# Performance work log

Hardware: AMD Instinct MI355X
Metric: run time of the kernel (lower is better)

Reference implementation:

```python
import jax, jax.numpy as jnp
import numpy as np

B, S, HID = 2, 2048, 2304
H, KVH, D = 8, 4, 256          # query heads, kv heads, head_dim
N_REP = H // KVH
SCALE = 256.0 ** -0.5          # query_pre_attn_scalar ** -0.5
SOFTCAP = 50.0
ROPE_THETA = 10000.0
NEG = -1e9


def setup_inputs() -> dict:
    key = jax.random.key(0)
    k1, k2, k3, k4, k5 = jax.random.split(key, 5)
    hidden_states = jax.random.normal(k1, (B, S, HID), dtype=jnp.float32)
    # RoPE cos/sin tables, shape [B, S, D]
    inv_freq = 1.0 / (ROPE_THETA ** (jnp.arange(0, D, 2, dtype=jnp.float32) / D))
    pos = jnp.arange(S, dtype=jnp.float32)
    freqs = pos[:, None] * inv_freq[None, :]            # [S, D/2]
    emb = jnp.concatenate([freqs, freqs], axis=-1)      # [S, D]
    cos = jnp.broadcast_to(jnp.cos(emb)[None], (B, S, D))
    sin = jnp.broadcast_to(jnp.sin(emb)[None], (B, S, D))
    # additive causal mask [B, 1, S, S] (sliding_window=4096 > S, so pure causal)
    idx = jnp.arange(S)
    causal = idx[None, :] <= idx[:, None]
    attention_mask = jnp.broadcast_to(
        jnp.where(causal, 0.0, NEG).astype(jnp.float32)[None, None], (B, 1, S, S))
    # projection weights (lecun-normal-ish scale), no bias (attention_bias=False)
    Wq = jax.random.normal(k2, (HID, H * D), dtype=jnp.float32) / np.sqrt(HID)
    Wk = jax.random.normal(k3, (HID, KVH * D), dtype=jnp.float32) / np.sqrt(HID)
    Wv = jax.random.normal(k4, (HID, KVH * D), dtype=jnp.float32) / np.sqrt(HID)
    Wo = jax.random.normal(k5, (H * D, HID), dtype=jnp.float32) / np.sqrt(H * D)
    return {"hidden_states": hidden_states, "cos": cos, "sin": sin,
            "attention_mask": attention_mask,
            "Wq": Wq, "Wk": Wk, "Wv": Wv, "Wo": Wo}


def _rotate_half(x):
    half = x.shape[-1] // 2
    return jnp.concatenate([-x[..., half:], x[..., :half]], axis=-1)


def reference(hidden_states, cos, sin, attention_mask, Wq, Wk, Wv, Wo):
    b, s, _ = hidden_states.shape
    q = (hidden_states @ Wq).reshape(b, s, H, D).transpose(0, 2, 1, 3)    # [B,H,S,D]
    k = (hidden_states @ Wk).reshape(b, s, KVH, D).transpose(0, 2, 1, 3)  # [B,KVH,S,D]
    v = (hidden_states @ Wv).reshape(b, s, KVH, D).transpose(0, 2, 1, 3)
    c = cos[:, None]  # [B,1,S,D] broadcast over heads (unsqueeze_dim=1)
    sn = sin[:, None]
    q = q * c + _rotate_half(q) * sn
    k = k * c + _rotate_half(k) * sn
    # GQA: repeat kv heads (interleave, matching repeat_kv tile+reshape)
    k = jnp.repeat(k, N_REP, axis=1)
    v = jnp.repeat(v, N_REP, axis=1)
    w = jnp.einsum('bhqd,bhkd->bhqk', q, k) * SCALE
    w = jnp.tanh(w / SOFTCAP) * SOFTCAP                  # logit softcapping
    w = w + attention_mask[:, :, :, :s]
    w = jax.nn.softmax(w.astype(jnp.float32), axis=-1).astype(q.dtype)
    out = jnp.einsum('bhqk,bhkd->bhqd', w, v)
    out = out.transpose(0, 2, 1, 3).reshape(b, s, H * D)
    return out @ Wo
```

## Files before the change

### kernel.cpp

```cpp
#include <hip/hip_runtime.h>

typedef unsigned short u16;
typedef __attribute__((ext_vector_type(8))) short short8;
typedef __attribute__((ext_vector_type(4))) float f32x4;

constexpr int B_ = 2;
constexpr int H_ = 8;
constexpr int KVH_ = 4;
constexpr int S_ = 2048;
constexpr int D_ = 256;
constexpr int HID_ = 2304;
constexpr int QKVN_ = 4096;
constexpr int AON_ = 2048;

__device__ __forceinline__ float b2f(u16 u) {
  union { float f; unsigned int i; } x; x.i = ((unsigned int)u) << 16; return x.f;
}
__device__ __forceinline__ u16 f2b(float f) {
  unsigned int x = __float_as_uint(f);
  unsigned int r = (x + 0x7fffu + ((x >> 16) & 1u)) >> 16;
  return (u16)r;
}

__global__ void cast_kernel(const float* __restrict__ in, u16* __restrict__ out) {
  size_t i = ((size_t)blockIdx.x * 256 + threadIdx.x) * 4;
  float4 v = *(const float4*)(in + i);
  unsigned int lo = (unsigned int)f2b(v.x) | ((unsigned int)f2b(v.y) << 16);
  unsigned int hi = (unsigned int)f2b(v.z) | ((unsigned int)f2b(v.w) << 16);
  uint2 o; o.x = lo; o.y = hi;
  *(uint2*)(out + i) = o;
}

__global__ void transpose_cast(const float* __restrict__ src, u16* __restrict__ dst,
                               int R, int C) {
  __shared__ float tile[64][65];
  int r0 = blockIdx.y * 64, c0 = blockIdx.x * 64;
  int t = threadIdx.x;
#pragma unroll
  for (int i = 0; i < 16; ++i) {
    int e = i * 256 + t;
    int r = e >> 6, c = e & 63;
    tile[r][c] = src[(size_t)(r0 + r) * C + (c0 + c)];
  }
  __syncthreads();
#pragma unroll
  for (int i = 0; i < 16; ++i) {
    int e = i * 256 + t;
    int orow = e >> 6, ocol = e & 63;
    dst[(size_t)(c0 + orow) * R + (r0 + ocol)] = f2b(tile[ocol][orow]);
  }
}

template <int OUTF32>
__global__ __launch_bounds__(256, 2) void gemm_bt(
    const u16* __restrict__ A, const u16* __restrict__ B, void* __restrict__ Cp,
    int M, int N, int K) {
  __shared__ u16 As[128 * 32];
  __shared__ u16 Bs[128 * 32];
  int m0 = blockIdx.y * 128, n0 = blockIdx.x * 128;
  int tid = threadIdx.x;
  int lane = tid & 63, wave = tid >> 6;
  int wy = wave >> 1, wx = wave & 1;
  int quad = lane >> 4, l16 = lane & 15;
  f32x4 acc[4][4] = {};
  for (int k0 = 0; k0 < K; k0 += 32) {
#pragma unroll
    for (int i = 0; i < 2; ++i) {
      int chunk = i * 256 + tid;
      int row = chunk >> 2, col = (chunk & 3) << 3;
      __builtin_amdgcn_global_load_lds(
          (const __attribute__((address_space(1))) void*)(A + (size_t)(m0 + row) * K + k0 + col),
          (__attribute__((address_space(3))) void*)(As + chunk * 8), 16, 0, 0);
    }
#pragma unroll
    for (int i = 0; i < 2; ++i) {
      int chunk = i * 256 + tid;
      int row = chunk >> 2, col = (chunk & 3) << 3;
      __builtin_amdgcn_global_load_lds(
          (const __attribute__((address_space(1))) void*)(B + (size_t)(n0 + row) * K + k0 + col),
          (__attribute__((address_space(3))) void*)(Bs + chunk * 8), 16, 0, 0);
    }
    __syncthreads();
    short8 af[4], bf[4];
#pragma unroll
    for (int mi = 0; mi < 4; ++mi)
      af[mi] = *(const short8*)(As + (wy * 64 + mi * 16 + l16) * 32 + quad * 8);
#pragma unroll
    for (int ni = 0; ni < 4; ++ni)
      bf[ni] = *(const short8*)(Bs + (wx * 64 + ni * 16 + l16) * 32 + quad * 8);
#pragma unroll
    for (int mi = 0; mi < 4; ++mi)
#pragma unroll
      for (int ni = 0; ni < 4; ++ni)
        acc[mi][ni] = __builtin_amdgcn_mfma_f32_16x16x32_bf16(af[mi], bf[ni], acc[mi][ni], 0, 0, 0);
    __syncthreads();
  }
#pragma unroll
  for (int mi = 0; mi < 4; ++mi) {
#pragma unroll
    for (int ni = 0; ni < 4; ++ni) {
#pragma unroll
      for (int r = 0; r < 4; ++r) {
        int row = m0 + wy * 64 + mi * 16 + quad * 4 + r;
        int col = n0 + wx * 64 + ni * 16 + l16;
        if (OUTF32)
          ((float*)Cp)[(size_t)row * N + col] = acc[mi][ni][r];
        else
          ((u16*)Cp)[(size_t)row * N + col] = f2b(acc[mi][ni][r]);
      }
    }
  }
}

__global__ void rope_kernel(const u16* __restrict__ qkv, const float* __restrict__ cs,
                            const float* __restrict__ sn, u16* __restrict__ Qr,
                            u16* __restrict__ Kr) {
  int row = blockIdx.x;
  int b = row >> 11, s = row & 2047;
  int d = threadIdx.x;
  const u16* qrow = qkv + (size_t)row * QKVN_;
  float c = cs[(size_t)row * D_ + d];
  float si = sn[(size_t)row * D_ + d];
  int dp = (d < 128) ? d + 128 : d - 128;
  float sgn = (d < 128) ? -1.f : 1.f;
#pragma unroll
  for (int h = 0; h < H_; ++h) {
    float v = b2f(qrow[h * D_ + d]);
    float p = sgn * b2f(qrow[h * D_ + dp]);
    Qr[((size_t)(b * H_ + h) * S_ + s) * D_ + d] = f2b(v * c + p * si);
  }
#pragma unroll
  for (int g = 0; g < KVH_; ++g) {
    float v = b2f(qrow[2048 + g * D_ + d]);
    float p = sgn * b2f(qrow[2048 + g * D_ + dp]);
    Kr[((size_t)(b * KVH_ + g) * S_ + s) * D_ + d] = f2b(v * c + p * si);
  }
}

__global__ void transpose_v(const u16* __restrict__ qkv, u16* __restrict__ Vt) {
  __shared__ u16 tile[64][72];
  int d0 = blockIdx.x * 64, s0 = blockIdx.y * 64, g = blockIdx.z;
  int b = g >> 2, kvh = g & 3;
  int t = threadIdx.x;
#pragma unroll
  for (int i = 0; i < 16; ++i) {
    int e = i * 256 + t;
    int r = e >> 6, c = e & 63;
    tile[r][c] = qkv[(size_t)(b * S_ + s0 + r) * QKVN_ + 3072 + kvh * D_ + d0 + c];
  }
  __syncthreads();
#pragma unroll
  for (int i = 0; i < 16; ++i) {
    int e = i * 256 + t;
    int orow = e >> 6, ocol = e & 63;
    Vt[((size_t)g * D_ + d0 + orow) * S_ + s0 + ocol] = tile[ocol][orow];
  }
}

__global__ __launch_bounds__(256, 2) void attn_kernel(
    const u16* __restrict__ Qr, const u16* __restrict__ Kr, const u16* __restrict__ Vt,
    u16* __restrict__ Ao) {
  __shared__ u16 Ks[32 * 256];
  __shared__ u16 Vs[256 * 32];
  __shared__ u16 Ps[4][16 * 40];
  int qt = 31 - blockIdx.x;
  int h = blockIdx.y, b = blockIdx.z;
  int kvh = h >> 1;
  int tid = threadIdx.x, wave = tid >> 6, lane = tid & 63;
  int quad = lane >> 4, l16 = lane & 15;
  int q0 = qt * 64;
  const u16* Qbase = Qr + ((size_t)(b * H_ + h) * S_ + q0 + wave * 16 + l16) * D_;
  short8 qf[8];
#pragma unroll
  for (int kk = 0; kk < 8; ++kk)
    qf[kk] = *(const short8*)(Qbase + kk * 32 + quad * 8);
  const u16* Kbase = Kr + (size_t)(b * KVH_ + kvh) * S_ * D_;
  const u16* Vbase = Vt + (size_t)(b * KVH_ + kvh) * D_ * S_;
  float l_r[4] = {0.f, 0.f, 0.f, 0.f};
  f32x4 o_acc[16] = {};
  int nkt = 2 * qt + 2;
  for (int kt = 0; kt < nkt; ++kt) {
    int k0 = kt * 32;
    __syncthreads();
#pragma unroll
    for (int i = 0; i < 4; ++i) {
      int p = i * 256 + tid;
      int s = p >> 5, pc = p & 31;
      int c = pc ^ (s & 7);
      __builtin_amdgcn_global_load_lds(
          (const __attribute__((address_space(1))) void*)(Kbase + (size_t)(k0 + s) * D_ + c * 8),
          (__attribute__((address_space(3))) void*)(Ks + p * 8), 16, 0, 0);
    }
#pragma unroll
    for (int i = 0; i < 4; ++i) {
      int p = i * 256 + tid;
      int d = p >> 2, ps = p & 3;
      int sl = ps ^ (d & 3);
      __builtin_amdgcn_global_load_lds(
          (const __attribute__((address_space(1))) void*)(Vbase + (size_t)d * S_ + k0 + sl * 8),
          (__attribute__((address_space(3))) void*)(Vs + p * 8), 16, 0, 0);
    }
    __syncthreads();
    f32x4 sacc[2] = {};
#pragma unroll
    for (int n = 0; n < 2; ++n) {
      int srow = n * 16 + l16;
      const u16* kb = Ks + srow * 256;
      int sw = l16 & 7;
#pragma unroll
      for (int kk = 0; kk < 8; ++kk) {
        int phys = (kk * 4 + quad) ^ sw;
        short8 bfr = *(const short8*)(kb + phys * 8);
        sacc[n] = __builtin_amdgcn_mfma_f32_16x16x32_bf16(qf[kk], bfr, sacc[n], 0, 0, 0);
      }
    }
    float e[2][4], rs[4];
#pragma unroll
    for (int r = 0; r < 4; ++r) rs[r] = 0.f;
#pragma unroll
    for (int n = 0; n < 2; ++n) {
      int key = k0 + n * 16 + l16;
#pragma unroll
      for (int r = 0; r < 4; ++r) {
        int qq = q0 + wave * 16 + quad * 4 + r;
        float x2 = sacc[n][r] * (2.0f * 0.0625f / 50.0f);
        x2 = fminf(fmaxf(x2, -30.f), 30.f);
        float E = __expf(x2);
        float s = 50.0f * (E - 1.0f) * __frcp_rn(E + 1.0f);
        s = (key <= qq) ? s : -1e30f;
        float ee = __expf(s - 50.0f);
        e[n][r] = ee;
        rs[r] += ee;
      }
    }
#pragma unroll
    for (int off = 1; off < 16; off <<= 1)
#pragma unroll
      for (int r = 0; r < 4; ++r)
        rs[r] += __shfl_xor(rs[r], off, 64);
#pragma unroll
    for (int r = 0; r < 4; ++r) l_r[r] += rs[r];
#pragma unroll
    for (int n = 0; n < 2; ++n)
#pragma unroll
      for (int r = 0; r < 4; ++r)
        Ps[wave][(quad * 4 + r) * 40 + n * 16 + l16] = f2b(e[n][r]);
    short8 pa = *(const short8*)(&Ps[wave][l16 * 40 + quad * 8]);
#pragma unroll
    for (int dt = 0; dt < 16; ++dt) {
      int d = dt * 16 + l16;
      int phys = quad ^ (d & 3);
      short8 vb = *(const short8*)(Vs + d * 32 + phys * 8);
      o_acc[dt] = __builtin_amdgcn_mfma_f32_16x16x32_bf16(pa, vb, o_acc[dt], 0, 0, 0);
    }
  }
#pragma unroll
  for (int r = 0; r < 4; ++r) l_r[r] = 1.0f / l_r[r];
#pragma unroll
  for (int dt = 0; dt < 16; ++dt)
#pragma unroll
    for (int r = 0; r < 4; ++r) {
      int row = b * S_ + q0 + wave * 16 + quad * 4 + r;
      int col = h * D_ + dt * 16 + l16;
      Ao[(size_t)row * AON_ + col] = f2b(o_acc[dt][r] * l_r[r]);
    }
}

extern "C" void kernel_launch(void* const* d_in, const int* in_sizes, int n_in,
                              void* d_out, int out_size, void* d_ws, size_t ws_size,
                              hipStream_t stream) {
  const float* hidden = (const float*)d_in[0];
  const float* cosp = (const float*)d_in[1];
  const float* sinp = (const float*)d_in[2];
  const float* Wq = (const float*)d_in[4];
  const float* Wk = (const float*)d_in[5];
  const float* Wv = (const float*)d_in[6];
  const float* Wo = (const float*)d_in[7];

  u16* hs  = (u16*)d_ws;
  u16* WT  = hs  + (size_t)4096 * HID_;
  u16* WoT = WT  + (size_t)4096 * HID_;
  u16* qkv = WoT + (size_t)HID_ * AON_;
  u16* Qr  = qkv + (size_t)4096 * QKVN_;
  u16* Kr  = Qr  + (size_t)B_ * H_ * S_ * D_;
  u16* Vt  = Kr  + (size_t)B_ * KVH_ * S_ * D_;
  u16* Ao  = Vt  + (size_t)B_ * KVH_ * S_ * D_;

  cast_kernel<<<9216, 256, 0, stream>>>(hidden, hs);
  transpose_cast<<<dim3(32, 36), 256, 0, stream>>>(Wq, WT, HID_, 2048);
  transpose_cast<<<dim3(16, 36), 256, 0, stream>>>(Wk, WT + (size_t)2048 * HID_, HID_, 1024);
  transpose_cast<<<dim3(16, 36), 256, 0, stream>>>(Wv, WT + (size_t)3072 * HID_, HID_, 1024);
  transpose_cast<<<dim3(36, 32), 256, 0, stream>>>(Wo, WoT, 2048, HID_);
  gemm_bt<0><<<dim3(32, 32), 256, 0, stream>>>(hs, WT, qkv, 4096, QKVN_, HID_);
  rope_kernel<<<4096, 256, 0, stream>>>(qkv, cosp, sinp, Qr, Kr);
  transpose_v<<<dim3(4, 32, 8), 256, 0, stream>>>(qkv, Vt);
  attn_kernel<<<dim3(32, 8, 2), 256, 0, stream>>>(Qr, Kr, Vt, Ao);
  gemm_bt<1><<<dim3(18, 32), 256, 0, stream>>>(Ao, WoT, d_out, 4096, HID_, 2048);
}
```

Before: 478.3 us.

## Raise attention occupancy, balance causal tiles, fix V swizzle, simplify softcap softmax

The attention kernel's launch bounds go from 2 to 4 blocks per SM, which tightens the register budget (the kernel holds a 64-float o_acc plus Q fragments). The query-tile order is reversed for batch 1 so that heavy and light causal tiles interleave across the grid. The V shared-memory XOR swizzle now uses (d>>1)&3 to reduce LDS bank conflicts. The tanh softcap plus fixed-max exp is algebraically folded into exp(-100/(E+1)), the causal mask is skipped for tiles fully below the diagonal, and P is written to LDS inline. The risks are register spills under the new bound and dropping the clamp on the exp argument.

```diff
diff --git a/kernel.cpp b/kernel.cpp
--- a/kernel.cpp
+++ b/kernel.cpp
@@ -157,14 +157,15 @@
   }
 }
 
-__global__ __launch_bounds__(256, 2) void attn_kernel(
+__global__ __launch_bounds__(256, 4) void attn_kernel(
     const u16* __restrict__ Qr, const u16* __restrict__ Kr, const u16* __restrict__ Vt,
     u16* __restrict__ Ao) {
   __shared__ u16 Ks[32 * 256];
   __shared__ u16 Vs[256 * 32];
   __shared__ u16 Ps[4][16 * 40];
-  int qt = 31 - blockIdx.x;
-  int h = blockIdx.y, b = blockIdx.z;
+  int b = blockIdx.z;
+  int qt = (b == 0) ? (31 - blockIdx.x) : blockIdx.x;
+  int h = blockIdx.y;
   int kvh = h >> 1;
   int tid = threadIdx.x, wave = tid >> 6, lane = tid & 63;
   int quad = lane >> 4, l16 = lane & 15;
@@ -195,7 +196,7 @@
     for (int i = 0; i < 4; ++i) {
       int p = i * 256 + tid;
       int d = p >> 2, ps = p & 3;
-      int sl = ps ^ (d & 3);
+      int sl = ps ^ ((d >> 1) & 3);
       __builtin_amdgcn_global_load_lds(
           (const __attribute__((address_space(1))) void*)(Vbase + (size_t)d * S_ + k0 + sl * 8),
           (__attribute__((address_space(3))) void*)(Vs + p * 8), 16, 0, 0);
@@ -214,23 +215,21 @@
         sacc[n] = __builtin_amdgcn_mfma_f32_16x16x32_bf16(qf[kk], bfr, sacc[n], 0, 0, 0);
       }
     }
-    float e[2][4], rs[4];
-#pragma unroll
-    for (int r = 0; r < 4; ++r) rs[r] = 0.f;
+    float rs[4] = {0.f, 0.f, 0.f, 0.f};
+    bool full = (k0 + 31 <= q0 + wave * 16);
 #pragma unroll
     for (int n = 0; n < 2; ++n) {
       int key = k0 + n * 16 + l16;
 #pragma unroll
       for (int r = 0; r < 4; ++r) {
-        int qq = q0 + wave * 16 + quad * 4 + r;
-        float x2 = sacc[n][r] * (2.0f * 0.0625f / 50.0f);
-        x2 = fminf(fmaxf(x2, -30.f), 30.f);
-        float E = __expf(x2);
-        float s = 50.0f * (E - 1.0f) * __frcp_rn(E + 1.0f);
-        s = (key <= qq) ? s : -1e30f;
-        float ee = __expf(s - 50.0f);
-        e[n][r] = ee;
+        float E = __expf(sacc[n][r] * 0.0025f);
+        float ee = __expf(-100.0f * __frcp_rn(E + 1.0f));
+        if (!full) {
+          int qq = q0 + wave * 16 + quad * 4 + r;
+          ee = (key <= qq) ? ee : 0.0f;
+        }
         rs[r] += ee;
+        Ps[wave][(quad * 4 + r) * 40 + n * 16 + l16] = f2b(ee);
       }
     }
 #pragma unroll
@@ -240,16 +239,11 @@
         rs[r] += __shfl_xor(rs[r], off, 64);
 #pragma unroll
     for (int r = 0; r < 4; ++r) l_r[r] += rs[r];
-#pragma unroll
-    for (int n = 0; n < 2; ++n)
-#pragma unroll
-      for (int r = 0; r < 4; ++r)
-        Ps[wave][(quad * 4 + r) * 40 + n * 16 + l16] = f2b(e[n][r]);
     short8 pa = *(const short8*)(&Ps[wave][l16 * 40 + quad * 8]);
 #pragma unroll
     for (int dt = 0; dt < 16; ++dt) {
       int d = dt * 16 + l16;
-      int phys = quad ^ (d & 3);
+      int phys = quad ^ ((d >> 1) & 3);
       short8 vb = *(const short8*)(Vs + d * 32 + phys * 8);
       o_acc[dt] = __builtin_amdgcn_mfma_f32_16x16x32_bf16(pa, vb, o_acc[dt], 0, 0, 0);
     }
```

After: 575.2 us. +20.3%, slower.
